# Kernel optimization log

Measured on AMD Instinct MI355X. Metric: run time of the kernel, lower is better.

The kernel has to match this reference:

```python
import jax, jax.numpy as jnp
import numpy as np

B, S, F_IN = 8, 2048, 1024
H, SC = 512, 256
N_LAYERS = 3


def _glorot(key, shape):
    fan_in, fan_out = shape[-2], shape[-1]
    lim = float(np.sqrt(6.0 / (fan_in + fan_out)))
    return jax.random.uniform(key, shape, jnp.float32, -lim, lim)


def setup_inputs() -> dict:
    key = jax.random.key(0)
    ks = jax.random.split(key, 8)
    x = jax.random.normal(ks[0], (B, S, F_IN), jnp.float32)
    Wp = _glorot(ks[1], (F_IN, H)); bp = jnp.zeros((H,), jnp.float32)
    gcn_W = _glorot(ks[2], (N_LAYERS, H, H)); gcn_b = jnp.zeros((N_LAYERS, H), jnp.float32)
    s1_W = _glorot(ks[3], (H, SC)); s1_b = jnp.zeros((SC,), jnp.float32)
    s2_W = _glorot(ks[4], (SC, SC // 2)); s2_b = jnp.zeros((SC // 2,), jnp.float32)
    s3_W = _glorot(ks[5], (SC // 2, 1)); s3_b = jnp.zeros((1,), jnp.float32)
    return {"x": x, "Wp": Wp, "bp": bp, "gcn_W": gcn_W, "gcn_b": gcn_b,
            "s1_W": s1_W, "s1_b": s1_b, "s2_W": s2_W, "s2_b": s2_b,
            "s3_W": s3_W, "s3_b": s3_b}


def _build_adj(seq_len):
    # tridiagonal band: self + immediate temporal neighbors
    a = jnp.eye(seq_len, dtype=jnp.float32)
    a = a + jnp.eye(seq_len, k=1, dtype=jnp.float32) + jnp.eye(seq_len, k=-1, dtype=jnp.float32)
    deg = a.sum(axis=1)
    dinv = jnp.power(deg + 1e-8, -0.5)
    # D^{-1/2} A D^{-1/2}
    return dinv[:, None] * a * dinv[None, :]


def reference(x, Wp, bp, gcn_W, gcn_b, s1_W, s1_b, s2_W, s2_b, s3_W, s3_b):
    seq_len = x.shape[1]
    adj = _build_adj(seq_len)  # [S, S]
    h = jnp.einsum('bsf,fh->bsh', x, Wp) + bp  # feature projection
    for i in range(N_LAYERS):
        support = jnp.einsum('bsh,hk->bsk', h, gcn_W[i])
        h = jnp.einsum('st,btk->bsk', adj, support) + gcn_b[i]
        if i < N_LAYERS - 1:
            h = jax.nn.relu(h)  # dropout is identity in eval mode
    z = jax.nn.relu(jnp.einsum('bsh,hc->bsc', h, s1_W) + s1_b)
    z = jax.nn.relu(jnp.einsum('bsc,cd->bsd', z, s2_W) + s2_b)
    scores = jax.nn.sigmoid(jnp.einsum('bsd,do->bso', z, s3_W) + s3_b)
    return scores[..., 0]  # [B, S]
```

## Files before the change

### kernel.cpp

```cpp
#include <hip/hip_runtime.h>
#include <hip/hip_fp16.h>
#include <cstdint>
#include <cstddef>


typedef _Float16 f16;
typedef _Float16 f16x8 __attribute__((ext_vector_type(8)));
typedef float    f32x4 __attribute__((ext_vector_type(4)));

__device__ __forceinline__ void async_cp16(const void* g, void* l) {
  __builtin_amdgcn_global_load_lds((const __attribute__((address_space(1))) void*)g,
                                   (__attribute__((address_space(3))) void*)l, 16, 0, 0);
}

__device__ __forceinline__ f16x8 splat8(f16 v) {
  f16x8 r;
#pragma unroll
  for (int e = 0; e < 8; ++e) r[e] = v;
  return r;
}

template<int BM, int BN, bool RELU, bool HAS_BIAS>
__global__ __launch_bounds__(512, 2) void proj_gemm_kernel(
    const float* __restrict__ Aptr, const f16* __restrict__ BT,
    f16* __restrict__ C, const float* __restrict__ bias,
    int M, int N, int K)
{
  constexpr int BK = 64;
  constexpr int NT = 512;
  constexpr int WAVES_N = 4;
  constexpr int WM = BM / 2;
  constexpr int WN = BN / WAVES_N;
  constexpr int TM = WM / 16;
  constexpr int TN = WN / 16;
  constexpr int ITER_B = (BN * BK) / (NT * 8);

  __shared__ __align__(16) f16 sA[2][BM * BK];
  __shared__ __align__(16) f16 sB[2][BN * BK];

  const int tid  = threadIdx.x;
  const int lane = tid & 63;
  const int wave = tid >> 6;
  const int wm   = wave / WAVES_N;
  const int wn   = wave % WAVES_N;
  const int m0   = blockIdx.x * BM;
  const int n0   = blockIdx.y * BN;
  const int quad = lane >> 4;
  const int l16  = lane & 15;

  uint32_t offA;
  {
    const int row = tid >> 3;
    const int q   = (tid & 7) ^ (row & 7);
    offA = (uint32_t)(((size_t)(m0 + row) * K + q * 8) * 4);
  }

  f32x4 acc[TM][TN];
#pragma unroll
  for (int i = 0; i < TM; ++i)
#pragma unroll
    for (int j = 0; j < TN; ++j)
      acc[i][j] = (f32x4){0.f, 0.f, 0.f, 0.f};

  float4 pa0, pa1;

  auto stageB = [&](int kt, int b) {
#pragma unroll
    for (int j = 0; j < ITER_B; ++j) {
      const int linear = j * NT + tid;
      const int row = linear >> 3;
      const int q   = (linear & 7) ^ (row & 7);
      async_cp16(BT + (size_t)(n0 + row) * K + kt + q * 8, &sB[b][linear * 8]);
    }
  };
  auto writeA = [&](int b) {
    f16x8 o;
    o[0] = (f16)pa0.x; o[1] = (f16)pa0.y; o[2] = (f16)pa0.z; o[3] = (f16)pa0.w;
    o[4] = (f16)pa1.x; o[5] = (f16)pa1.y; o[6] = (f16)pa1.z; o[7] = (f16)pa1.w;
    *(f16x8*)&sA[b][(size_t)tid * 8] = o;
  };
  auto compute = [&](int b) {
#pragma unroll
    for (int kk = 0; kk < 2; ++kk) {
      const int c = quad + kk * 4;
      f16x8 af[TM], bf[TN];
#pragma unroll
      for (int mi = 0; mi < TM; ++mi) {
        const int ml = wm * WM + mi * 16 + l16;
        af[mi] = *(const f16x8*)&sA[b][ml * 64 + ((c ^ (ml & 7)) * 8)];
      }
#pragma unroll
      for (int ni = 0; ni < TN; ++ni) {
        const int nl = wn * WN + ni * 16 + l16;
        bf[ni] = *(const f16x8*)&sB[b][nl * 64 + ((c ^ (nl & 7)) * 8)];
      }
#pragma unroll
      for (int mi = 0; mi < TM; ++mi)
#pragma unroll
        for (int ni = 0; ni < TN; ++ni)
          acc[mi][ni] = __builtin_amdgcn_mfma_f32_16x16x32_f16(
              af[mi], bf[ni], acc[mi][ni], 0, 0, 0);
    }
  };

  {
    const float4* p = (const float4*)((const char*)Aptr + offA);
    pa0 = p[0]; pa1 = p[1];
  }
  stageB(0, 0);
  writeA(0);
  __syncthreads();

  const int nt = K / BK;
  for (int t = 0; t < nt; ++t) {
    const int cur = t & 1;
    const bool pf = (t + 1 < nt);
    if (pf) {
      const float4* p = (const float4*)((const char*)Aptr + (size_t)(t + 1) * BK * 4 + offA);
      pa0 = p[0]; pa1 = p[1];
      stageB((t + 1) * BK, cur ^ 1);
    }
    compute(cur);
    if (pf) writeA(cur ^ 1);
    __syncthreads();
  }

#pragma unroll
  for (int ni = 0; ni < TN; ++ni) {
    const int nc = n0 + wn * WN + ni * 16 + l16;
    const float bv = HAS_BIAS ? bias[nc] : 0.0f;
#pragma unroll
    for (int mi = 0; mi < TM; ++mi) {
#pragma unroll
      for (int r = 0; r < 4; ++r) {
        const int mr = m0 + wm * WM + mi * 16 + quad * 4 + r;
        float v = acc[mi][ni][r] + bv;
        if (RELU) v = fmaxf(v, 0.0f);
        C[(size_t)mr * N + nc] = (f16)v;
      }
    }
  }
}

template<bool RELU>
__global__ __launch_bounds__(256, 2) void gcn_gemm_kernel(
    const f16* __restrict__ hin, const f16* __restrict__ WT,
    f16* __restrict__ C, const float* __restrict__ bias, int M)
{
  constexpr int BM = 128, BN = 128, BK = 64;
  constexpr int NT = 256;
  constexpr int TM = 4, TN = 4;
  constexpr int S = 2048, H = 512;
  constexpr int AROWS = BM + 2;

  __shared__ __align__(16) f16 sA[2][AROWS * BK];
  __shared__ __align__(16) f16 sB[2][BN * BK];

  const int tid  = threadIdx.x;
  const int lane = tid & 63;
  const int wave = tid >> 6;
  const int wm   = wave >> 1;
  const int wn   = wave & 1;
  const int quad = lane >> 4;
  const int l16  = lane & 15;
  const int m0   = blockIdx.x * BM;
  const int n0   = blockIdx.y * BN;

  const float dM = 0.57735026919f;
  const float dE = 0.70710678118f;

  f16 cf[TM][3];
#pragma unroll
  for (int mi = 0; mi < TM; ++mi) {
    const int grow = m0 + wm * 64 + mi * 16 + l16;
    const int s = grow & (S - 1);
    const float dsv = (s == 0 || s == S - 1) ? dE : dM;
    cf[mi][0] = (f16)((s > 0)     ? dsv * ((s - 1 == 0) ? dE : dM)     : 0.0f);
    cf[mi][1] = (f16)(dsv * dsv);
    cf[mi][2] = (f16)((s < S - 1) ? dsv * ((s + 1 == S - 1) ? dE : dM) : 0.0f);
  }

  const int h_row = (tid >> 3) ? (BM + 1) : 0;
  const int h_i   = tid & 7;
  const int h_q   = h_i ^ (h_row & 7);
  int hg = m0 - 1 + h_row;
  hg = hg < 0 ? 0 : (hg >= M ? M - 1 : hg);
  f16x8 h_v;

  auto halo_load = [&](int kt) {
    if (tid < 16) h_v = *(const f16x8*)(hin + (size_t)hg * H + kt + h_q * 8);
  };
  auto halo_write = [&](int b) {
    if (tid < 16) *(f16x8*)&sA[b][(size_t)(h_row * 8 + h_i) * 8] = h_v;
  };
  auto stage_glds = [&](int kt, int b) {
#pragma unroll
    for (int j = 0; j < 4; ++j) {
      const int linear = j * NT + tid;
      const int row = linear >> 3;
      const int q   = (linear & 7) ^ (row & 7);
      async_cp16(WT + (size_t)(n0 + row) * H + kt + q * 8, &sB[b][linear * 8]);
    }
#pragma unroll
    for (int j = 0; j < 4; ++j) {
      const int chunk = j * NT + tid + 8;
      const int row = chunk >> 3;
      const int q   = (chunk & 7) ^ (row & 7);
      async_cp16(hin + (size_t)(m0 + row - 1) * H + kt + q * 8, &sA[b][chunk * 8]);
    }
  };

  f32x4 acc[TM][TN];
#pragma unroll
  for (int i = 0; i < TM; ++i)
#pragma unroll
    for (int j = 0; j < TN; ++j)
      acc[i][j] = (f32x4){0.f, 0.f, 0.f, 0.f};

  auto compute = [&](int b) {
#pragma unroll
    for (int kk = 0; kk < 2; ++kk) {
      const int c = quad + kk * 4;
      f16x8 af[TM], bf[TN];
#pragma unroll
      for (int mi = 0; mi < TM; ++mi) {
        const int ldr = wm * 64 + mi * 16 + l16 + 1;
        f16x8 pv = *(const f16x8*)&sA[b][(ldr - 1) * 64 + ((c ^ ((ldr - 1) & 7)) * 8)];
        f16x8 sv = *(const f16x8*)&sA[b][(ldr    ) * 64 + ((c ^ ((ldr    ) & 7)) * 8)];
        f16x8 nv = *(const f16x8*)&sA[b][(ldr + 1) * 64 + ((c ^ ((ldr + 1) & 7)) * 8)];
        f16x8 r = pv * splat8(cf[mi][0]);
        r += sv * splat8(cf[mi][1]);
        r += nv * splat8(cf[mi][2]);
        af[mi] = r;
      }
#pragma unroll
      for (int ni = 0; ni < TN; ++ni) {
        const int nl = wn * 64 + ni * 16 + l16;
        bf[ni] = *(const f16x8*)&sB[b][nl * 64 + ((c ^ (nl & 7)) * 8)];
      }
#pragma unroll
      for (int mi = 0; mi < TM; ++mi)
#pragma unroll
        for (int ni = 0; ni < TN; ++ni)
          acc[mi][ni] = __builtin_amdgcn_mfma_f32_16x16x32_f16(
              af[mi], bf[ni], acc[mi][ni], 0, 0, 0);
    }
  };

  halo_load(0);
  stage_glds(0, 0);
  halo_write(0);
  __syncthreads();

  constexpr int NTILES = H / BK;
  for (int t = 0; t < NTILES; ++t) {
    const int cur = t & 1;
    const bool pf = (t + 1 < NTILES);
    if (pf) {
      halo_load((t + 1) * BK);
      stage_glds((t + 1) * BK, cur ^ 1);
    }
    compute(cur);
    if (pf) halo_write(cur ^ 1);
    __syncthreads();
  }

#pragma unroll
  for (int ni = 0; ni < TN; ++ni) {
    const int nc = n0 + wn * 64 + ni * 16 + l16;
    const float bv = bias[nc];
#pragma unroll
    for (int mi = 0; mi < TM; ++mi) {
#pragma unroll
      for (int r = 0; r < 4; ++r) {
        const int mr = m0 + wm * 64 + mi * 16 + quad * 4 + r;
        float v = acc[mi][ni][r] + bv;
        if (RELU) v = fmaxf(v, 0.0f);
        C[(size_t)mr * H + nc] = (f16)v;
      }
    }
  }
}

__global__ __launch_bounds__(256) void head_fused_kernel(
    const f16* __restrict__ h, const f16* __restrict__ S1T,
    const f16* __restrict__ S2T,
    const float* __restrict__ s1b, const float* __restrict__ s2b,
    const float* __restrict__ s3w, const float* __restrict__ s3b,
    float* __restrict__ out)
{
  __shared__ __align__(16) char smem[36864 + 32 * 264 * 2];
  f16* sA  = (f16*)smem;
  f16* sB  = (f16*)(smem + 4096);
  f16* zs  = (f16*)(smem + 36864);
  f16* z2s = (f16*)smem;
  f16* sB2 = (f16*)(smem + 8704);

  const int tid  = threadIdx.x;
  const int lane = tid & 63;
  const int wave = tid >> 6;
  const int quad = lane >> 4;
  const int l16  = lane & 15;
  const int m0   = blockIdx.x * 32;

  f32x4 acc[2][4];
#pragma unroll
  for (int i = 0; i < 2; ++i)
#pragma unroll
    for (int j = 0; j < 4; ++j) acc[i][j] = (f32x4){0.f, 0.f, 0.f, 0.f};

  for (int kt = 0; kt < 512; kt += 64) {
    __syncthreads();
    {
      const int linear = tid;
      const int row = linear >> 3;
      const int q   = (linear & 7) ^ (row & 7);
      async_cp16(h + (size_t)(m0 + row) * 512 + kt + q * 8, &sA[linear * 8]);
    }
#pragma unroll
    for (int j = 0; j < 8; ++j) {
      const int linear = j * 256 + tid;
      const int row = linear >> 3;
      const int q   = (linear & 7) ^ (row & 7);
      async_cp16(S1T + (size_t)row * 512 + kt + q * 8, &sB[linear * 8]);
    }
    __syncthreads();
#pragma unroll
    for (int kk = 0; kk < 2; ++kk) {
      const int c = quad + kk * 4;
      f16x8 af[2], bf[4];
#pragma unroll
      for (int mi = 0; mi < 2; ++mi) {
        const int ml = mi * 16 + l16;
        af[mi] = *(const f16x8*)&sA[ml * 64 + ((c ^ (ml & 7)) * 8)];
      }
#pragma unroll
      for (int ni = 0; ni < 4; ++ni) {
        const int nl = wave * 64 + ni * 16 + l16;
        bf[ni] = *(const f16x8*)&sB[nl * 64 + ((c ^ (nl & 7)) * 8)];
      }
#pragma unroll
      for (int mi = 0; mi < 2; ++mi)
#pragma unroll
        for (int ni = 0; ni < 4; ++ni)
          acc[mi][ni] = __builtin_amdgcn_mfma_f32_16x16x32_f16(
              af[mi], bf[ni], acc[mi][ni], 0, 0, 0);
    }
  }
#pragma unroll
  for (int ni = 0; ni < 4; ++ni) {
    const int nc = wave * 64 + ni * 16 + l16;
    const float bv = s1b[nc];
#pragma unroll
    for (int mi = 0; mi < 2; ++mi)
#pragma unroll
      for (int r = 0; r < 4; ++r) {
        const int row = mi * 16 + quad * 4 + r;
        zs[row * 264 + nc] = (f16)fmaxf(acc[mi][ni][r] + bv, 0.0f);
      }
  }
  __syncthreads();

  f32x4 acc2[2][2];
#pragma unroll
  for (int i = 0; i < 2; ++i)
#pragma unroll
    for (int j = 0; j < 2; ++j) acc2[i][j] = (f32x4){0.f, 0.f, 0.f, 0.f};

  for (int kt2 = 0; kt2 < 4; ++kt2) {
    __syncthreads();
#pragma unroll
    for (int j = 0; j < 4; ++j) {
      const int linear = j * 256 + tid;
      const int row = linear >> 3;
      const int q   = (linear & 7) ^ (row & 7);
      async_cp16(S2T + (size_t)row * 256 + kt2 * 64 + q * 8, &sB2[linear * 8]);
    }
    __syncthreads();
#pragma unroll
    for (int kk = 0; kk < 2; ++kk) {
      const int c = quad + kk * 4;
      f16x8 af[2], bf[2];
#pragma unroll
      for (int mi = 0; mi < 2; ++mi) {
        const int row = mi * 16 + l16;
        af[mi] = *(const f16x8*)&zs[row * 264 + (kt2 * 8 + c) * 8];
      }
#pragma unroll
      for (int ni = 0; ni < 2; ++ni) {
        const int nl = wave * 32 + ni * 16 + l16;
        bf[ni] = *(const f16x8*)&sB2[nl * 64 + ((c ^ (nl & 7)) * 8)];
      }
#pragma unroll
      for (int mi = 0; mi < 2; ++mi)
#pragma unroll
        for (int ni = 0; ni < 2; ++ni)
          acc2[mi][ni] = __builtin_amdgcn_mfma_f32_16x16x32_f16(
              af[mi], bf[ni], acc2[mi][ni], 0, 0, 0);
    }
  }
  __syncthreads();
#pragma unroll
  for (int ni = 0; ni < 2; ++ni) {
    const int nc = wave * 32 + ni * 16 + l16;
    const float bv = s2b[nc];
#pragma unroll
    for (int mi = 0; mi < 2; ++mi)
#pragma unroll
      for (int r = 0; r < 4; ++r) {
        const int row = mi * 16 + quad * 4 + r;
        z2s[row * 136 + nc] = (f16)fmaxf(acc2[mi][ni][r] + bv, 0.0f);
      }
  }
  __syncthreads();

  const int m  = tid >> 3;
  const int qd = tid & 7;
  float p = 0.f;
#pragma unroll
  for (int j = 0; j < 2; ++j) {
    f16x8 v = *(const f16x8*)&z2s[m * 136 + qd * 16 + j * 8];
#pragma unroll
    for (int e = 0; e < 8; ++e) p += (float)v[e] * s3w[qd * 16 + j * 8 + e];
  }
  p += __shfl_xor(p, 1);
  p += __shfl_xor(p, 2);
  p += __shfl_xor(p, 4);
  if (qd == 0) out[m0 + m] = 1.0f / (1.0f + expf(-(p + s3b[0])));
}

__global__ __launch_bounds__(256) void prep_kernel(
    const float* __restrict__ Wp, f16* __restrict__ WpT,
    const float* __restrict__ gW, f16* __restrict__ GT,
    const float* __restrict__ s1W, f16* __restrict__ S1T,
    const float* __restrict__ s2W, f16* __restrict__ S2T)
{
  __shared__ f16 s[64 * 68];
  const int tid = threadIdx.x;
  int b = blockIdx.x;

  const float* W; f16* WT; int K, N, tile;
  if (b < 128)      { W = Wp;  WT = WpT; K = 1024; N = 512; tile = b; }
  else if (b < 320) { const int i = (b - 128) >> 6;
                      W = gW + (size_t)i * 262144; WT = GT + (size_t)i * 262144;
                      K = 512; N = 512; tile = (b - 128) & 63; }
  else if (b < 352) { W = s1W; WT = S1T; K = 512; N = 256; tile = b - 320; }
  else              { W = s2W; WT = S2T; K = 256; N = 128; tile = b - 352; }

  const int nt = tile % (N >> 6);
  const int kt = tile / (N >> 6);
#pragma unroll
  for (int it = 0; it < 16; ++it) {
    const int i  = it * 256 + tid;
    const int rk = i >> 6, rn = i & 63;
    s[rn * 68 + rk] = (f16)W[(size_t)(kt * 64 + rk) * N + nt * 64 + rn];
  }
  __syncthreads();
#pragma unroll
  for (int it = 0; it < 16; ++it) {
    const int i  = it * 256 + tid;
    const int rn = i >> 6, rk = i & 63;
    WT[(size_t)(nt * 64 + rn) * K + kt * 64 + rk] = s[rn * 68 + rk];
  }
}

extern "C" void kernel_launch(void* const* d_in, const int* in_sizes, int n_in,
                              void* d_out, int out_size, void* d_ws, size_t ws_size,
                              hipStream_t stream) {
  (void)in_sizes; (void)n_in; (void)out_size; (void)ws_size;
  const float* x   = (const float*)d_in[0];
  const float* Wp  = (const float*)d_in[1];
  const float* bp  = (const float*)d_in[2];
  const float* gW  = (const float*)d_in[3];
  const float* gb  = (const float*)d_in[4];
  const float* s1W = (const float*)d_in[5];
  const float* s1b = (const float*)d_in[6];
  const float* s2W = (const float*)d_in[7];
  const float* s2b = (const float*)d_in[8];
  const float* s3W = (const float*)d_in[9];
  const float* s3b = (const float*)d_in[10];
  float* out = (float*)d_out;

  constexpr int M = 16384;
  char* ws = (char*)d_ws;
  f16* hA  = (f16*)(ws + 0);
  f16* hB  = (f16*)(ws + 16777216);
  f16* WpT = (f16*)(ws + 33554432);
  f16* GT  = (f16*)(ws + 34603008);
  f16* S1T = (f16*)(ws + 36175872);
  f16* S2T = (f16*)(ws + 36438016);

  prep_kernel<<<360, 256, 0, stream>>>(Wp, WpT, gW, GT, s1W, S1T, s2W, S2T);

  proj_gemm_kernel<64, 256, false, true>
      <<<dim3(M / 64, 2), 512, 0, stream>>>(x, WpT, hA, bp, M, 512, 1024);

  gcn_gemm_kernel<true>
      <<<dim3(M / 128, 4), 256, 0, stream>>>(hA, GT, hB, gb, M);
  gcn_gemm_kernel<true>
      <<<dim3(M / 128, 4), 256, 0, stream>>>(hB, GT + 262144, hA, gb + 512, M);
  gcn_gemm_kernel<false>
      <<<dim3(M / 128, 4), 256, 0, stream>>>(hA, GT + 524288, hB, gb + 1024, M);

  head_fused_kernel<<<M / 32, 256, 0, stream>>>(hB, S1T, S2T, s1b, s2b, s3W, s3b, out);
}
```

Measured before the change: 198.6 us.

## Stream halo rows via async LDS loads and use partial vmcnt waits

Replaces the register-staged halo load/write with direct global_load_lds copies issued by every wave, precomputes clamped global offsets once outside the K loop, and swaps __syncthreads for explicit s_waitcnt vmcnt(9) plus s_barrier. The aim is to let the next tile's loads stay in flight while the current tile is computed and to drop per-iteration address arithmetic and the extra LDS store. The risk is that the hand-counted vmcnt value and the raw barriers are fragile: a wrong count or a compiler reordering could cause races. Every wave now also issues its own halo copy into the same LDS slots, so those writes are duplicated.

```diff
diff --git a/kernel.cpp b/kernel.cpp
--- a/kernel.cpp
+++ b/kernel.cpp
@@ -180,34 +180,41 @@
     cf[mi][2] = (f16)((s < S - 1) ? dsv * ((s + 1 == S - 1) ? dE : dM) : 0.0f);
   }
 
-  const int h_row = (tid >> 3) ? (BM + 1) : 0;
-  const int h_i   = tid & 7;
-  const int h_q   = h_i ^ (h_row & 7);
-  int hg = m0 - 1 + h_row;
-  hg = hg < 0 ? 0 : (hg >= M ? M - 1 : hg);
-  f16x8 h_v;
-
-  auto halo_load = [&](int kt) {
-    if (tid < 16) h_v = *(const f16x8*)(hin + (size_t)hg * H + kt + h_q * 8);
-  };
-  auto halo_write = [&](int b) {
-    if (tid < 16) *(f16x8*)&sA[b][(size_t)(h_row * 8 + h_i) * 8] = h_v;
-  };
-  auto stage_glds = [&](int kt, int b) {
-#pragma unroll
-    for (int j = 0; j < 4; ++j) {
-      const int linear = j * NT + tid;
-      const int row = linear >> 3;
-      const int q   = (linear & 7) ^ (row & 7);
-      async_cp16(WT + (size_t)(n0 + row) * H + kt + q * 8, &sB[b][linear * 8]);
-    }
-#pragma unroll
-    for (int j = 0; j < 4; ++j) {
-      const int chunk = j * NT + tid + 8;
-      const int row = chunk >> 3;
-      const int q   = (chunk & 7) ^ (row & 7);
-      async_cp16(hin + (size_t)(m0 + row - 1) * H + kt + q * 8, &sA[b][chunk * 8]);
-    }
+  uint32_t offB[4], offA[4], offH;
+#pragma unroll
+  for (int j = 0; j < 4; ++j) {
+    const int linear = j * NT + tid;
+    const int row = linear >> 3;
+    const int q   = (linear & 7) ^ (row & 7);
+    offB[j] = (uint32_t)((size_t)(n0 + row) * H + q * 8);
+  }
+#pragma unroll
+  for (int j = 0; j < 4; ++j) {
+    const int c = j * NT + tid;
+    const int r = c >> 3;
+    const int q = (c & 7) ^ (r & 7);
+    int g = m0 - 1 + r;
+    g = g < 0 ? 0 : (g >= M ? M - 1 : g);
+    offA[j] = (uint32_t)((size_t)g * H + q * 8);
+  }
+  {
+    const int c = 1024 + (lane & 15);
+    const int r = c >> 3;
+    const int q = (c & 7) ^ (r & 7);
+    int g = m0 - 1 + r;
+    g = g < 0 ? 0 : (g >= M ? M - 1 : g);
+    offH = (uint32_t)((size_t)g * H + q * 8);
+  }
+
+  auto stage = [&](int kt, int b) {
+#pragma unroll
+    for (int j = 0; j < 4; ++j)
+      async_cp16(WT + (size_t)offB[j] + kt, &sB[b][(j * NT + tid) * 8]);
+#pragma unroll
+    for (int j = 0; j < 4; ++j)
+      async_cp16(hin + (size_t)offA[j] + kt, &sA[b][(j * NT + tid) * 8]);
+    if (lane < 16)
+      async_cp16(hin + (size_t)offH + kt, &sA[b][(1024 + lane) * 8]);
   };
 
   f32x4 acc[TM][TN];
@@ -247,22 +254,20 @@
     }
   };
 
-  halo_load(0);
-  stage_glds(0, 0);
-  halo_write(0);
-  __syncthreads();
-
+  stage(0, 0);
   constexpr int NTILES = H / BK;
   for (int t = 0; t < NTILES; ++t) {
     const int cur = t & 1;
-    const bool pf = (t + 1 < NTILES);
-    if (pf) {
-      halo_load((t + 1) * BK);
-      stage_glds((t + 1) * BK, cur ^ 1);
-    }
+    if (t + 1 < NTILES) {
+      stage((t + 1) * BK, cur ^ 1);
+      asm volatile("s_waitcnt vmcnt(9)" ::: "memory");
+    } else {
+      asm volatile("s_waitcnt vmcnt(0)" ::: "memory");
+    }
+    asm volatile("s_barrier" ::: "memory");
+    __builtin_amdgcn_sched_barrier(0);
     compute(cur);
-    if (pf) halo_write(cur ^ 1);
-    __syncthreads();
+    asm volatile("s_barrier" ::: "memory");
   }
 
 #pragma unroll
```

After: 198.6 us. About the same (-0.0%).
